# Performance work log

Hardware: AMD Instinct MI355X
Metric: run time of the kernel (lower is better)

Reference implementation:

```python
import jax, jax.numpy as jnp
import numpy as np

BATCH, SEQ, HIDDEN = 2, 4096, 4096
HEADS, HEAD_DIM, BLOCK = 32, 128, 256
LAYER_IDX, N_LAYERS = 1, 32
EPS = 1e-5


def setup_inputs() -> dict:
    key = jax.random.key(0)
    ks = jax.random.split(key, 5)
    s = 0.02
    return {
        "hidden_states": jax.random.normal(ks[0], (BATCH, SEQ, HIDDEN), jnp.float32),
        "qkv_w": jax.random.normal(ks[1], (3 * HEADS * HEAD_DIM, HIDDEN), jnp.float32) * s,
        "out_w": jax.random.normal(ks[2], (HIDDEN, HEADS * HEAD_DIM), jnp.float32) * s,
        "gate_w": jax.random.normal(ks[3], (HEADS * HEAD_DIM, HIDDEN), jnp.float32) * s,
        "norm_w": jnp.ones((HEADS * HEAD_DIM,), jnp.float32),
    }


def _decays():
    # slope_rate: (h,1,1)
    base = 1.0 / 2.0 ** (8.0 / HEADS)
    exponent = jnp.arange(HEADS, dtype=jnp.float32) + 1.0
    factor = 1.0 - LAYER_IDX / (N_LAYERS - 1 + 1e-5) + 1e-5
    slope = (base ** exponent * factor)[:, None, None]
    r = jnp.arange(BLOCK, dtype=jnp.float32) + 1.0
    q_decay = jnp.exp(-slope * r[:, None])                 # (h, block, 1)
    k_decay = jnp.exp(-slope * (BLOCK - r)[:, None])       # (h, block, 1)
    diff = r[:, None] - r[None, :]                         # (block, block): i - j
    diag = slope[None] * diff[None, None]                  # (1, h, block, block)
    diag = jnp.where(diag >= 0, -diag, -jnp.inf)
    diag_decay = jnp.exp(diag)                             # causal intra-block decay
    block_decay = jnp.exp(-slope * BLOCK)                  # (h,1,1)
    return q_decay, k_decay, diag_decay, block_decay


def reference(hidden_states, qkv_w, out_w, gate_w, norm_w):
    b, s, _ = hidden_states.shape
    h, d, bs = HEADS, HEAD_DIM, BLOCK
    nb = s // bs
    q_decay, k_decay, diag_decay, block_decay = _decays()

    # qkv projection + silu, split per-head into q,k,v
    qkv = jax.nn.silu(hidden_states @ qkv_w.T)             # (b,s,3hd)
    qkv = qkv.reshape(b, s, h, 3, d)
    q = jnp.moveaxis(qkv[:, :, :, 0], 2, 1)                # (b,h,s,d)
    k = jnp.moveaxis(qkv[:, :, :, 1], 2, 1)
    v = jnp.moveaxis(qkv[:, :, :, 2], 2, 1)

    # split sequence into blocks, scan leading axis = block index
    def to_blocks(x):
        return jnp.moveaxis(x.reshape(b, h, nb, bs, d), 2, 0)  # (nb,b,h,bs,d)

    qb, kb, vb = to_blocks(q), to_blocks(k), to_blocks(v)

    def step(kv, blk):
        cq, ck, cv = blk
        # intra-block quadratic attention with causal decay
        scores = jnp.einsum('bhnd,bhmd->bhnm', cq, ck) * diag_decay
        intra = jnp.einsum('bhnm,bhmd->bhnd', scores, cv)
        # inter-block via decayed recurrent state kv: (b,h,d,d)
        inter = jnp.einsum('bhnd,bhde->bhne', cq * q_decay, kv)
        kv_next = kv * block_decay + jnp.einsum('bhnd,bhne->bhde', ck * k_decay, cv)
        return kv_next, intra + inter

    kv0 = jnp.zeros((b, h, d, d), hidden_states.dtype)
    _, out_blocks = jax.lax.scan(step, kv0, (qb, kb, vb))  # (nb,b,h,bs,d)

    attn = jnp.moveaxis(out_blocks, 0, 2)                  # (b,h,nb,bs,d)
    attn = attn.reshape(b, h, s, d).transpose(0, 2, 1, 3).reshape(b, s, h * d)

    # RMSNorm (fp32 accumulation, as MixtralRMSNorm)
    xf = attn.astype(jnp.float32)
    xf = xf * jax.lax.rsqrt(jnp.mean(xf * xf, axis=-1, keepdims=True) + EPS)
    normed = norm_w * xf.astype(attn.dtype)

    gate = jax.nn.sigmoid(hidden_states @ gate_w.T)
    return (gate * normed) @ out_w.T
```

## Files before the change

### kernel.cpp

```cpp
#include <hip/hip_runtime.h>

typedef unsigned short u16;
typedef __attribute__((ext_vector_type(4))) float f32x4;
typedef __attribute__((ext_vector_type(8))) __bf16 bf16x8;

#define SEQ   4096
#define HID   4096
#define HID3  12288

__device__ __forceinline__ float bf2f(u16 u){
  union { unsigned int i; float f; } v; v.i = ((unsigned int)u) << 16; return v.f;
}
__device__ __forceinline__ u16 f2bf(float f){
  union { float f; unsigned int i; } v; v.f = f;
  unsigned int r = (v.i + 0x7FFFu + ((v.i >> 16) & 1u)) >> 16;
  return (u16)r;
}
__device__ __forceinline__ float slope_of(int h){
  const float factor = 1.0f - 1.0f/(31.0f + 1e-5f) + 1e-5f;
  return exp2f(-0.25f * (float)(h + 1)) * factor;
}
__device__ __forceinline__ bf16x8 ld_bf8(const u16* p){
  return __builtin_bit_cast(bf16x8, *(const uint4*)p);
}
__device__ __forceinline__ void gload_lds16(const u16* g, u16* l){
  __builtin_amdgcn_global_load_lds((const __attribute__((address_space(1))) void*)g,
                                   (__attribute__((address_space(3))) void*)l, 16, 0, 0);
}

__global__ __launch_bounds__(256) void cvt_kernel(const float* __restrict__ in,
                                                  u16* __restrict__ out, long n){
  long i = ((long)blockIdx.x * 256 + threadIdx.x) * 4;
  long stride = (long)gridDim.x * 1024;
  for (; i < n; i += stride){
    float4 v = *(const float4*)(in + i);
    ushort4 o;
    o.x = f2bf(v.x); o.y = f2bf(v.y); o.z = f2bf(v.z); o.w = f2bf(v.w);
    *(ushort4*)(out + i) = o;
  }
}

template<int EPI>
__global__ __launch_bounds__(512) void gemm256(
    const u16* __restrict__ A, const u16* __restrict__ B, void* __restrict__ C,
    const u16* __restrict__ Aux, int M, int N, int K)
{
  __shared__ u16 ring[5][16384];
  const int t = threadIdx.x;
  const int w = t >> 6, l = t & 63, lr = l & 15, lk = l >> 4;
  const int mw = w >> 2, nw = w & 3;
  const int nbn = N >> 8;
  int nwg = gridDim.x;
  int bid = blockIdx.x;
  int bswz = (bid & 7) * (nwg >> 3) + (bid >> 3);
  int bm = bswz / nbn, bn = bswz % nbn;
  const u16* Abase = A + (long)(bm * 256) * K;
  const u16* Bbase = B + (long)(bn * 256) * K;
  const int NT = K >> 6;

  int sr[2], sku[2];
#pragma unroll
  for (int i = 0; i < 2; ++i){
    int dr = i * 64 + (t >> 3);
    int ul = (t & 7) ^ (dr & 7);
    sr[i]  = 2 * dr + (ul >> 2);
    sku[i] = ul & 3;
  }
  int offA[8], offB[4];
#pragma unroll
  for (int fn = 0; fn < 8; ++fn){
    int row = mw * 128 + fn * 16 + lr;
    offA[fn] = (row >> 1) * 64 + (((((row & 1) << 2) + lk) ^ ((row >> 1) & 7)) << 3);
  }
#pragma unroll
  for (int fe = 0; fe < 4; ++fe){
    int row = nw * 64 + fe * 16 + lr;
    offB[fe] = (row >> 1) * 64 + (((((row & 1) << 2) + lk) ^ ((row >> 1) & 7)) << 3);
  }

  auto stageA = [&](int kt, int c, int slot, int i){
    gload_lds16(Abase + (long)sr[i] * K + kt * 64 + c * 32 + sku[i] * 8,
                &ring[slot][i * 4096 + w * 512]);
  };
  auto stageB = [&](int kt, int c, int slot, int i){
    gload_lds16(Bbase + (long)sr[i] * K + kt * 64 + c * 32 + sku[i] * 8,
                &ring[slot][8192 + i * 4096 + w * 512]);
  };

  f32x4 acc[8][4] = {};

  stageA(0,0,0,0); stageA(0,0,0,1); stageB(0,0,0,0); stageB(0,0,0,1);
  stageA(0,1,1,0); stageA(0,1,1,1); stageB(0,1,1,0); stageB(0,1,1,1);
  if (1 < NT){ stageA(1,0,2,0); stageA(1,0,2,1); stageB(1,0,2,0); stageB(1,0,2,1); }
  asm volatile("s_waitcnt vmcnt(4)" ::: "memory");
  __builtin_amdgcn_s_barrier();

  int sa = 0;
  for (int p = 0; p < NT; ++p){
    int sb = sa + 1; if (sb >= 5) sb -= 5;
    int sx = sa + 3; if (sx >= 5) sx -= 5;
    int sy = sa + 4; if (sy >= 5) sy -= 5;
    const u16* Aa = &ring[sa][0];
    const u16* Ab = &ring[sb][0];
    const u16* Ba = &ring[sa][8192];
    const u16* Bb = &ring[sb][8192];
    bf16x8 bh[4][2];
#pragma unroll
    for (int q = 0; q < 4; ++q){
      bf16x8 af[2][2];
#pragma unroll
      for (int fnl = 0; fnl < 2; ++fnl){
        af[fnl][0] = ld_bf8(Aa + offA[q * 2 + fnl]);
        af[fnl][1] = ld_bf8(Ab + offA[q * 2 + fnl]);
      }
      if (q == 0){
#pragma unroll
        for (int fe = 0; fe < 4; ++fe){
          bh[fe][0] = ld_bf8(Ba + offB[fe]);
          bh[fe][1] = ld_bf8(Bb + offB[fe]);
        }
      }
      if (q == 0 && p + 1 < NT){ stageA(p+1, 1, sx, 0); stageA(p+1, 1, sx, 1); }
      if (q == 1 && p + 1 < NT){ stageB(p+1, 1, sx, 0); stageB(p+1, 1, sx, 1); }
      if (q == 2 && p + 2 < NT){ stageA(p+2, 0, sy, 0); stageA(p+2, 0, sy, 1); }
      if (q == 3 && p + 2 < NT){ stageB(p+2, 0, sy, 0); stageB(p+2, 0, sy, 1); }
      if (q == 0) asm volatile("s_waitcnt lgkmcnt(8)" ::: "memory");
      __builtin_amdgcn_s_barrier();
      asm volatile("s_waitcnt lgkmcnt(0)" ::: "memory");
      __builtin_amdgcn_sched_barrier(0);
      __builtin_amdgcn_s_setprio(1);
#pragma unroll
      for (int fnl = 0; fnl < 2; ++fnl)
#pragma unroll
        for (int fe = 0; fe < 4; ++fe){
          acc[q*2+fnl][fe] = __builtin_amdgcn_mfma_f32_16x16x32_bf16(af[fnl][0], bh[fe][0], acc[q*2+fnl][fe], 0, 0, 0);
          acc[q*2+fnl][fe] = __builtin_amdgcn_mfma_f32_16x16x32_bf16(af[fnl][1], bh[fe][1], acc[q*2+fnl][fe], 0, 0, 0);
        }
      __builtin_amdgcn_s_setprio(0);
      if (q == 3){
        if (p + 2 < NT) asm volatile("s_waitcnt vmcnt(4)" ::: "memory");
        else            asm volatile("s_waitcnt vmcnt(0)" ::: "memory");
      }
      __builtin_amdgcn_s_barrier();
    }
    sa += 2; if (sa >= 5) sa -= 5;
  }

  long crow = (long)bm * 256 + mw * 128 + lk * 4;
  long ccol = (long)bn * 256 + nw * 64 + lr;
#pragma unroll
  for (int fn = 0; fn < 8; ++fn)
#pragma unroll
    for (int fe = 0; fe < 4; ++fe)
#pragma unroll
      for (int reg = 0; reg < 4; ++reg){
        long row = crow + fn * 16 + reg;
        long col = ccol + fe * 16;
        float x = acc[fn][fe][reg];
        if (EPI == 0){
          ((u16*)C)[row * N + col] = f2bf(x / (1.0f + __expf(-x)));
        } else if (EPI == 1){
          float g = 1.0f / (1.0f + __expf(-x));
          ((u16*)C)[row * N + col] = f2bf(g * bf2f(Aux[row * N + col]));
        } else {
          ((float*)C)[row * N + col] = x;
        }
      }
}

__global__ __launch_bounds__(256) void attn_contrib(
    const u16* __restrict__ qkv, float* __restrict__ ct)
{
  __shared__ u16 kb[256 * 128];
  __shared__ u16 vb[256 * 128];
  __shared__ float kdec[256];
  int wg = blockIdx.x;
  int bh = wg >> 4, blk = wg & 15;
  int b = bh >> 5, h = bh & 31;
  int t = threadIdx.x;
  float slope = slope_of(h);
  kdec[t] = __expf(-slope * (float)(255 - t));
  const u16* kg = qkv + ((long)(b * SEQ + blk * 256)) * HID3 + h * 384 + 128;
  const u16* vg = kg + 128;
#pragma unroll
  for (int i = 0; i < 16; ++i){
    int chunk = t + i * 256;
    int row = chunk >> 4, c8 = (chunk & 15) << 3;
    *(uint4*)&kb[row * 128 + c8] = *(const uint4*)&kg[(long)row * HID3 + c8];
    *(uint4*)&vb[row * 128 + c8] = *(const uint4*)&vg[(long)row * HID3 + c8];
  }
  __syncthreads();
  int e0 = (t >> 4) << 3, d0 = (t & 15) << 3;
  float acc[8][8];
#pragma unroll
  for (int i = 0; i < 8; ++i)
#pragma unroll
    for (int j = 0; j < 8; ++j) acc[i][j] = 0.f;
  for (int n = 0; n < 256; ++n){
    float kd = kdec[n];
    uint4 vv = *(const uint4*)&vb[n * 128 + e0];
    uint4 kk = *(const uint4*)&kb[n * 128 + d0];
    const u16* vs = (const u16*)&vv;
    const u16* ks = (const u16*)&kk;
    float ve[8], kf[8];
#pragma unroll
    for (int x = 0; x < 8; ++x){ ve[x] = bf2f(vs[x]); kf[x] = bf2f(ks[x]) * kd; }
#pragma unroll
    for (int i = 0; i < 8; ++i)
#pragma unroll
      for (int j = 0; j < 8; ++j) acc[i][j] += ve[i] * kf[j];
  }
  float* out = ct + (long)wg * 16384;
#pragma unroll
  for (int i = 0; i < 8; ++i){
    *(float4*)&out[(e0 + i) * 128 + d0]     = make_float4(acc[i][0], acc[i][1], acc[i][2], acc[i][3]);
    *(float4*)&out[(e0 + i) * 128 + d0 + 4] = make_float4(acc[i][4], acc[i][5], acc[i][6], acc[i][7]);
  }
}

__global__ __launch_bounds__(256) void attn_scan(const float* __restrict__ ct,
                                                 u16* __restrict__ stTb)
{
  int bh = blockIdx.x, t = threadIdx.x;
  float bdec = __expf(-slope_of(bh & 31) * 256.0f);
  float cur[64];
#pragma unroll
  for (int i = 0; i < 64; ++i) cur[i] = 0.f;
  const float* base = ct + (long)bh * 16 * 16384;
  u16* ob = stTb + (long)bh * 16 * 16384;
  for (int blkI = 0; blkI < 16; ++blkI){
    const float* p = base + (long)blkI * 16384;
    u16* o = ob + (long)blkI * 16384;
#pragma unroll
    for (int i = 0; i < 64; ++i){
      o[t + i * 256] = f2bf(cur[i]);
      cur[i] = cur[i] * bdec + p[t + i * 256];
    }
  }
}

__global__ __launch_bounds__(512) void attn_mfma(
    const u16* __restrict__ qkv, const u16* __restrict__ stTb, u16* __restrict__ attn)
{
  __shared__ u16 Ks[256 * 130];
  __shared__ u16 VTs[128 * 258];
  __shared__ u16 Ps[4][64 * 34];
  int wg = blockIdx.x;
  int bh = wg >> 4, blk = wg & 15;
  int b = bh >> 5, h = bh & 31;
  int t = threadIdx.x;
  int w = t >> 6, l = t & 63, lr = l & 15, lk = l >> 4;
  int r = w >> 1, c = w & 1;
  float slope = slope_of(h);
  const u16* qg = qkv + ((long)(b * SEQ + blk * 256)) * HID3 + h * 384;
  const u16* kg = qg + 128;
  const u16* vg = qg + 256;

#pragma unroll
  for (int i = 0; i < 8; ++i){
    int chunk = t + i * 512;
    int row = chunk >> 4, c8 = (chunk & 15) << 3;
    *(uint4*)&Ks[row * 130 + c8] = *(const uint4*)&kg[(long)row * HID3 + c8];
    uint4 vv = *(const uint4*)&vg[(long)row * HID3 + c8];
    const u16* vs = (const u16*)&vv;
#pragma unroll
    for (int x = 0; x < 8; ++x) VTs[(c8 + x) * 258 + row] = vs[x];
  }
  bf16x8 qa[4][4];
#pragma unroll
  for (int fn = 0; fn < 4; ++fn)
#pragma unroll
    for (int kc = 0; kc < 4; ++kc)
      qa[fn][kc] = ld_bf8(&qg[(long)(r * 64 + fn * 16 + lr) * HID3 + kc * 32 + lk * 8]);
  f32x4 acc[4][4] = {};
  __syncthreads();

  int mtmax = 2 * r + 1;
  for (int mt = 0; mt < 8; ++mt){
    if (mt <= mtmax){
      f32x4 S[4] = {};
      int mrow = mt * 32 + c * 16 + lr;
      bf16x8 kb[4];
#pragma unroll
      for (int kc = 0; kc < 4; ++kc)
        kb[kc] = ld_bf8(&Ks[mrow * 130 + kc * 32 + lk * 8]);
#pragma unroll
      for (int fn = 0; fn < 4; ++fn)
#pragma unroll
        for (int kc = 0; kc < 4; ++kc)
          S[fn] = __builtin_amdgcn_mfma_f32_16x16x32_bf16(qa[fn][kc], kb[kc], S[fn], 0, 0, 0);
      int m = mt * 32 + c * 16 + lr;
#pragma unroll
      for (int fn = 0; fn < 4; ++fn)
#pragma unroll
        for (int reg = 0; reg < 4; ++reg){
          int n = r * 64 + fn * 16 + lk * 4 + reg;
          float dv = (n >= m) ? __expf(-slope * (float)(n - m)) : 0.f;
          Ps[r][(fn * 16 + lk * 4 + reg) * 34 + c * 16 + lr] = f2bf(S[fn][reg] * dv);
        }
    }
    __syncthreads();
    if (mt <= mtmax){
      bf16x8 pa[4], vb[4];
#pragma unroll
      for (int fn = 0; fn < 4; ++fn)
        pa[fn] = ld_bf8(&Ps[r][(fn * 16 + lr) * 34 + lk * 8]);
#pragma unroll
      for (int fe = 0; fe < 4; ++fe)
        vb[fe] = ld_bf8(&VTs[(c * 64 + fe * 16 + lr) * 258 + mt * 32 + lk * 8]);
#pragma unroll
      for (int fn = 0; fn < 4; ++fn)
#pragma unroll
        for (int fe = 0; fe < 4; ++fe)
          acc[fn][fe] = __builtin_amdgcn_mfma_f32_16x16x32_bf16(pa[fn], vb[fe], acc[fn][fe], 0, 0, 0);
    }
    __syncthreads();
  }

#pragma unroll
  for (int fn = 0; fn < 4; ++fn){
    int n = r * 64 + fn * 16 + lr;
    float qd = __expf(-slope * (float)(n + 1));
#pragma unroll
    for (int kc = 0; kc < 4; ++kc){
      union { bf16x8 v; u16 u[8]; } uu; uu.v = qa[fn][kc];
#pragma unroll
      for (int x = 0; x < 8; ++x) uu.u[x] = f2bf(bf2f(uu.u[x]) * qd);
      qa[fn][kc] = uu.v;
    }
  }
  const u16* sg = stTb + (long)(bh * 16 + blk) * 16384;
#pragma unroll
  for (int kc = 0; kc < 4; ++kc){
    bf16x8 sb2[4];
#pragma unroll
    for (int fe = 0; fe < 4; ++fe)
      sb2[fe] = ld_bf8(&sg[(c * 64 + fe * 16 + lr) * 128 + kc * 32 + lk * 8]);
#pragma unroll
    for (int fn = 0; fn < 4; ++fn)
#pragma unroll
      for (int fe = 0; fe < 4; ++fe)
        acc[fn][fe] = __builtin_amdgcn_mfma_f32_16x16x32_bf16(qa[fn][kc], sb2[fe], acc[fn][fe], 0, 0, 0);
  }

  u16* arow = attn + ((long)(b * SEQ + blk * 256)) * HID + h * 128;
#pragma unroll
  for (int fn = 0; fn < 4; ++fn)
#pragma unroll
    for (int fe = 0; fe < 4; ++fe)
#pragma unroll
      for (int reg = 0; reg < 4; ++reg){
        int n = r * 64 + fn * 16 + lk * 4 + reg;
        int col = c * 64 + fe * 16 + lr;
        arow[(long)n * HID + col] = f2bf(acc[fn][fe][reg]);
      }
}

__global__ __launch_bounds__(256) void rmsnorm_ip(u16* __restrict__ attn,
                                                  const float* __restrict__ nw)
{
  __shared__ float wsum[4];
  int row = blockIdx.x, t = threadIdx.x;
  u16* p = attn + (long)row * HID;
  uint4 v0 = *(const uint4*)&p[t * 8];
  uint4 v1 = *(const uint4*)&p[t * 8 + 2048];
  const u16* a0 = (const u16*)&v0;
  const u16* a1 = (const u16*)&v1;
  float f0[8], f1[8];
  float ss = 0.f;
#pragma unroll
  for (int x = 0; x < 8; ++x){
    f0[x] = bf2f(a0[x]); f1[x] = bf2f(a1[x]);
    ss += f0[x] * f0[x] + f1[x] * f1[x];
  }
#pragma unroll
  for (int off = 32; off > 0; off >>= 1) ss += __shfl_down(ss, off);
  if ((t & 63) == 0) wsum[t >> 6] = ss;
  __syncthreads();
  float rs = rsqrtf((wsum[0] + wsum[1] + wsum[2] + wsum[3]) * (1.0f / 4096.0f) + 1e-5f);
  alignas(16) u16 o0[8], o1[8];
#pragma unroll
  for (int x = 0; x < 8; ++x){
    o0[x] = f2bf(f0[x] * rs * nw[t * 8 + x]);
    o1[x] = f2bf(f1[x] * rs * nw[t * 8 + 2048 + x]);
  }
  *(uint4*)&p[t * 8]        = *(const uint4*)&o0[0];
  *(uint4*)&p[t * 8 + 2048] = *(const uint4*)&o1[0];
}

extern "C" void kernel_launch(void* const* d_in, const int* in_sizes, int n_in,
                              void* d_out, int out_size, void* d_ws, size_t ws_size,
                              hipStream_t stream)
{
  const float* hidden = (const float*)d_in[0];
  const float* qkv_w  = (const float*)d_in[1];
  const float* out_w  = (const float*)d_in[2];
  const float* gate_w = (const float*)d_in[3];
  const float* norm_w = (const float*)d_in[4];
  char* ws = (char*)d_ws;
  const long SZ_X  = 67108864L;
  const long SZ_WQ = 100663296L;
  const long SZ_WG = 33554432L;
  const long SZ_WO = 33554432L;
  const long SZ_QA = 201326592L;
  const long SZ_AT = 67108864L;
  u16* Xb   = (u16*)(ws);
  u16* Wq   = (u16*)(ws + SZ_X);
  u16* Wg   = (u16*)(ws + SZ_X + SZ_WQ);
  u16* Wo   = (u16*)(ws + SZ_X + SZ_WQ + SZ_WG);
  u16* qact = (u16*)(ws + SZ_X + SZ_WQ + SZ_WG + SZ_WO);
  u16* attn = (u16*)(ws + SZ_X + SZ_WQ + SZ_WG + SZ_WO + SZ_QA);
  float* st   = (float*)Wq;
  u16*   stTb = (u16*)(ws + SZ_X + 67108864L);
  u16* gated = qact;
  if (ws_size < (size_t)(SZ_X + SZ_WQ + SZ_WG + SZ_WO + SZ_QA + SZ_AT)) return;

  cvt_kernel<<<1024, 256, 0, stream>>>(hidden, Xb, 33554432L);
  cvt_kernel<<<1024, 256, 0, stream>>>(qkv_w,  Wq, 50331648L);
  cvt_kernel<<<1024, 256, 0, stream>>>(gate_w, Wg, 16777216L);
  cvt_kernel<<<1024, 256, 0, stream>>>(out_w,  Wo, 16777216L);

  gemm256<0><<<32 * 48, 512, 0, stream>>>(Xb, Wq, (void*)qact, nullptr, 8192, 12288, 4096);

  attn_contrib<<<1024, 256, 0, stream>>>(qact, st);
  attn_scan<<<64, 256, 0, stream>>>(st, stTb);
  attn_mfma<<<1024, 512, 0, stream>>>(qact, stTb, attn);
  rmsnorm_ip<<<8192, 256, 0, stream>>>(attn, norm_w);

  gemm256<1><<<32 * 16, 512, 0, stream>>>(Xb, Wg, (void*)gated, attn, 8192, 4096, 4096);
  gemm256<2><<<32 * 16, 512, 0, stream>>>(gated, Wo, d_out, nullptr, 8192, 4096, 4096);
}
```

Baseline: 1.903 ms.

## Hoist GEMM LDS A-fragment loads, drop per-quarter barriers, split scan across more blocks

The GEMM main loop now reads all A fragments from LDS early, in the first three quarter-steps. It also removes the two barriers per quarter, keeping one barrier per K-tile after the vmcnt wait, which cuts synchronisation stalls and gives more overlap between LDS reads and MFMA. Separately, the state scan is split four ways across the d*d state, giving 256 blocks with 16 registers each instead of 64 blocks with 64 registers each, for more parallelism. Removing the per-quarter barriers risks LDS hazards if the ring slot being staged overlaps slots still being read. More live A fragments also raise register pressure.

```diff
diff --git a/kernel.cpp b/kernel.cpp
--- a/kernel.cpp
+++ b/kernel.cpp
@@ -104,45 +104,59 @@
     const u16* Ab = &ring[sb][0];
     const u16* Ba = &ring[sa][8192];
     const u16* Bb = &ring[sb][8192];
-    bf16x8 bh[4][2];
+    bf16x8 bh[4][2], af[4][2][2];
 #pragma unroll
     for (int q = 0; q < 4; ++q){
-      bf16x8 af[2][2];
-#pragma unroll
-      for (int fnl = 0; fnl < 2; ++fnl){
-        af[fnl][0] = ld_bf8(Aa + offA[q * 2 + fnl]);
-        af[fnl][1] = ld_bf8(Ab + offA[q * 2 + fnl]);
-      }
       if (q == 0){
 #pragma unroll
         for (int fe = 0; fe < 4; ++fe){
           bh[fe][0] = ld_bf8(Ba + offB[fe]);
           bh[fe][1] = ld_bf8(Bb + offB[fe]);
         }
+#pragma unroll
+        for (int fnl = 0; fnl < 2; ++fnl){
+          af[0][fnl][0] = ld_bf8(Aa + offA[fnl]);
+          af[0][fnl][1] = ld_bf8(Ab + offA[fnl]);
+        }
+#pragma unroll
+        for (int fnl = 0; fnl < 2; ++fnl){
+          af[1][fnl][0] = ld_bf8(Aa + offA[2 + fnl]);
+          af[1][fnl][1] = ld_bf8(Ab + offA[2 + fnl]);
+        }
+        if (p + 1 < NT){ stageA(p+1, 1, sx, 0); stageA(p+1, 1, sx, 1); }
+      } else if (q == 1){
+#pragma unroll
+        for (int fnl = 0; fnl < 2; ++fnl){
+          af[2][fnl][0] = ld_bf8(Aa + offA[4 + fnl]);
+          af[2][fnl][1] = ld_bf8(Ab + offA[4 + fnl]);
+        }
+        if (p + 1 < NT){ stageB(p+1, 1, sx, 0); stageB(p+1, 1, sx, 1); }
+      } else if (q == 2){
+#pragma unroll
+        for (int fnl = 0; fnl < 2; ++fnl){
+          af[3][fnl][0] = ld_bf8(Aa + offA[6 + fnl]);
+          af[3][fnl][1] = ld_bf8(Ab + offA[6 + fnl]);
+        }
+        if (p + 2 < NT){ stageA(p+2, 0, sy, 0); stageA(p+2, 0, sy, 1); }
+      } else {
+        if (p + 2 < NT){ stageB(p+2, 0, sy, 0); stageB(p+2, 0, sy, 1); }
       }
-      if (q == 0 && p + 1 < NT){ stageA(p+1, 1, sx, 0); stageA(p+1, 1, sx, 1); }
-      if (q == 1 && p + 1 < NT){ stageB(p+1, 1, sx, 0); stageB(p+1, 1, sx, 1); }
-      if (q == 2 && p + 2 < NT){ stageA(p+2, 0, sy, 0); stageA(p+2, 0, sy, 1); }
-      if (q == 3 && p + 2 < NT){ stageB(p+2, 0, sy, 0); stageB(p+2, 0, sy, 1); }
-      if (q == 0) asm volatile("s_waitcnt lgkmcnt(8)" ::: "memory");
-      __builtin_amdgcn_s_barrier();
-      asm volatile("s_waitcnt lgkmcnt(0)" ::: "memory");
+      if (q < 3) asm volatile("s_waitcnt lgkmcnt(4)" ::: "memory");
+      else       asm volatile("s_waitcnt lgkmcnt(0)" ::: "memory");
       __builtin_amdgcn_sched_barrier(0);
       __builtin_amdgcn_s_setprio(1);
 #pragma unroll
       for (int fnl = 0; fnl < 2; ++fnl)
 #pragma unroll
         for (int fe = 0; fe < 4; ++fe){
-          acc[q*2+fnl][fe] = __builtin_amdgcn_mfma_f32_16x16x32_bf16(af[fnl][0], bh[fe][0], acc[q*2+fnl][fe], 0, 0, 0);
-          acc[q*2+fnl][fe] = __builtin_amdgcn_mfma_f32_16x16x32_bf16(af[fnl][1], bh[fe][1], acc[q*2+fnl][fe], 0, 0, 0);
+          acc[q*2+fnl][fe] = __builtin_amdgcn_mfma_f32_16x16x32_bf16(af[q][fnl][0], bh[fe][0], acc[q*2+fnl][fe], 0, 0, 0);
+          acc[q*2+fnl][fe] = __builtin_amdgcn_mfma_f32_16x16x32_bf16(af[q][fnl][1], bh[fe][1], acc[q*2+fnl][fe], 0, 0, 0);
         }
       __builtin_amdgcn_s_setprio(0);
-      if (q == 3){
-        if (p + 2 < NT) asm volatile("s_waitcnt vmcnt(4)" ::: "memory");
-        else            asm volatile("s_waitcnt vmcnt(0)" ::: "memory");
-      }
-      __builtin_amdgcn_s_barrier();
     }
+    if (p + 2 < NT) asm volatile("s_waitcnt vmcnt(4)" ::: "memory");
+    else            asm volatile("s_waitcnt vmcnt(0)" ::: "memory");
+    __builtin_amdgcn_s_barrier();
     sa += 2; if (sa >= 5) sa -= 5;
   }
 
@@ -221,18 +235,20 @@
 __global__ __launch_bounds__(256) void attn_scan(const float* __restrict__ ct,
                                                  u16* __restrict__ stTb)
 {
-  int bh = blockIdx.x, t = threadIdx.x;
+  int g = blockIdx.x;
+  int bh = g >> 2, sl = g & 3;
+  int t = threadIdx.x;
   float bdec = __expf(-slope_of(bh & 31) * 256.0f);
-  float cur[64];
-#pragma unroll
-  for (int i = 0; i < 64; ++i) cur[i] = 0.f;
-  const float* base = ct + (long)bh * 16 * 16384;
-  u16* ob = stTb + (long)bh * 16 * 16384;
+  float cur[16];
+#pragma unroll
+  for (int i = 0; i < 16; ++i) cur[i] = 0.f;
+  const float* base = ct + (long)bh * 16 * 16384 + sl * 4096;
+  u16* ob = stTb + (long)bh * 16 * 16384 + sl * 4096;
   for (int blkI = 0; blkI < 16; ++blkI){
     const float* p = base + (long)blkI * 16384;
     u16* o = ob + (long)blkI * 16384;
 #pragma unroll
-    for (int i = 0; i < 64; ++i){
+    for (int i = 0; i < 16; ++i){
       o[t + i * 256] = f2bf(cur[i]);
       cur[i] = cur[i] * bdec + p[t + i * 256];
     }
@@ -423,7 +439,7 @@
   gemm256<0><<<32 * 48, 512, 0, stream>>>(Xb, Wq, (void*)qact, nullptr, 8192, 12288, 4096);
 
   attn_contrib<<<1024, 256, 0, stream>>>(qact, st);
-  attn_scan<<<64, 256, 0, stream>>>(st, stTb);
+  attn_scan<<<256, 256, 0, stream>>>(st, stTb);
   attn_mfma<<<1024, 512, 0, stream>>>(qact, stTb, attn);
   rmsnorm_ip<<<8192, 256, 0, stream>>>(attn, norm_w);
 
```

New measurement: 1.699 ms. -10.7%, faster.
